# Kernel tuning notes

Measured on AMD Instinct MI355X. Metric: run time of the kernel, lower is better.

Reference implementation:

```python
import jax, jax.numpy as jnp
import numpy as np

N_NODES = 100000
N_EDGES = 1600000
D_FEAT = 64
NUM_LAYERS = 3


def setup_inputs() -> dict:
    key = jax.random.key(0)
    k1, k2, k3, k4 = jax.random.split(key, 4)
    X = jax.random.normal(k1, (N_NODES, D_FEAT), dtype=jnp.float32)
    src = jax.random.randint(k2, (N_EDGES,), 0, N_NODES, dtype=jnp.int32)
    dst = jax.random.randint(k3, (N_EDGES,), 0, N_NODES, dtype=jnp.int32)
    ew = jax.random.uniform(k4, (N_EDGES,), dtype=jnp.float32)
    return {"X": X, "src": src, "dst": dst, "ew": ew}


def _spmm(X, src, dst, ew):
    # gather source features, scale by edge weight, scatter-sum into dst
    msgs = X[src] * ew[:, None]  # [E, d]
    return jax.ops.segment_sum(msgs, dst, num_segments=N_NODES)


def reference(X, src, dst, ew):
    # LightGCNConv with stack_layers=True: average of layer-0..num_layers embeddings
    X_list = [X]
    h = X
    for _ in range(NUM_LAYERS):
        h = _spmm(h, src, dst, ew)
        X_list.append(h)
    return jnp.mean(jnp.stack(X_list, axis=1), axis=1)  # [N, d]
```

## Files before the change

kernel.cpp:

```cpp
#include <hip/hip_runtime.h>
#include <hip/hip_fp16.h>

#define N_NODES 100000
#define D_FEAT  64
#define N_EDGES 1600000
#define NPB     128
#define NBUCK   ((N_NODES + NPB - 1) / NPB)
#define CAP     3072
#define CVT_BLOCKS  500
#define CVT_THREADS 1024
#define CHUNK   (N_EDGES / CVT_BLOCKS)
#define PULL_BLOCKS 2048
#define WCAP    64

__global__ void init_bcur(int* __restrict__ bcur) {
    int t = threadIdx.x;
    if (t < NBUCK) bcur[t] = 0;
}

__global__ __launch_bounds__(CVT_THREADS) void cvt_part(const float* __restrict__ X,
                                                        __half* __restrict__ Xh,
                                                        const int* __restrict__ src,
                                                        const int* __restrict__ dst,
                                                        const float* __restrict__ ew,
                                                        int* __restrict__ bcur,
                                                        int2* __restrict__ edges_p) {
    __shared__ int h[NBUCK];
    const int t = threadIdx.x;
    for (int i = t; i < NBUCK; i += CVT_THREADS) h[i] = 0;

    const int n4 = N_NODES * D_FEAT / 4;
    for (int i = blockIdx.x * CVT_THREADS + t; i < n4; i += CVT_BLOCKS * CVT_THREADS) {
        float4 v = ((const float4*)X)[i];
        ((__half2*)Xh)[2 * i]     = __floats2half2_rn(v.x, v.y);
        ((__half2*)Xh)[2 * i + 1] = __floats2half2_rn(v.z, v.w);
    }
    __syncthreads();

    const int beg = blockIdx.x * CHUNK;
    const int base = beg + 4 * t;
    const bool act = (4 * t < CHUNK);

    int4 d4;
    if (act) {
        d4 = *(const int4*)(dst + base);
        atomicAdd(&h[d4.x >> 7], 1);
        atomicAdd(&h[d4.y >> 7], 1);
        atomicAdd(&h[d4.z >> 7], 1);
        atomicAdd(&h[d4.w >> 7], 1);
    }
    __syncthreads();

    if (t < NBUCK) {
        int c = h[t];
        h[t] = c ? atomicAdd(&bcur[t], c) : 0;
    }
    __syncthreads();

    if (act) {
        int4   s4 = *(const int4*)(src + base);
        float4 w4 = *(const float4*)(ew + base);
        int b, p;
        b = d4.x >> 7; p = atomicAdd(&h[b], 1);
        if (p < CAP) edges_p[(size_t)b * CAP + p] = make_int2(s4.x | ((d4.x & 127) << 17), __float_as_int(w4.x));
        b = d4.y >> 7; p = atomicAdd(&h[b], 1);
        if (p < CAP) edges_p[(size_t)b * CAP + p] = make_int2(s4.y | ((d4.y & 127) << 17), __float_as_int(w4.y));
        b = d4.z >> 7; p = atomicAdd(&h[b], 1);
        if (p < CAP) edges_p[(size_t)b * CAP + p] = make_int2(s4.z | ((d4.z & 127) << 17), __float_as_int(w4.z));
        b = d4.w >> 7; p = atomicAdd(&h[b], 1);
        if (p < CAP) edges_p[(size_t)b * CAP + p] = make_int2(s4.w | ((d4.w & 127) << 17), __float_as_int(w4.w));
    }
}

__global__ __launch_bounds__(256) void sort_bucket(const int2* __restrict__ edges_p,
                                                   const int* __restrict__ bcur,
                                                   int2* __restrict__ sedges,
                                                   int2* __restrict__ nodeptr) {
    __shared__ int cnt[NPB], sc[NPB], cur[NPB];
    __shared__ int2 buf[CAP];
    const int b = blockIdx.x, t = threadIdx.x;
    const int beg = b * CAP;
    int n = bcur[b];
    if (n > CAP) n = CAP;

    if (t < NPB) cnt[t] = 0;
    __syncthreads();
    for (int i = t; i < n; i += 256) {
        int2 e = edges_p[beg + i];
        buf[i] = e;
        atomicAdd(&cnt[e.x >> 17], 1);
    }
    __syncthreads();

    if (t < NPB) sc[t] = cnt[t];
    __syncthreads();
    for (int off = 1; off < NPB; off <<= 1) {
        int v = (t >= off && t < NPB) ? sc[t - off] : 0;
        __syncthreads();
        if (t < NPB) sc[t] += v;
        __syncthreads();
    }
    if (t < NPB) {
        cur[t] = sc[t] - cnt[t];
        int node = b * NPB + t;
        if (node < N_NODES) nodeptr[node] = make_int2(beg + sc[t] - cnt[t], cnt[t]);
    }
    __syncthreads();

    for (int i = t; i < n; i += 256) {
        int2 e = buf[i];
        int p = atomicAdd(&cur[e.x >> 17], 1);
        sedges[beg + p] = make_int2((e.x & 0x1FFFF) << 7, e.y);
    }
}

template <int MODE>
__global__ __launch_bounds__(256) void spmm_pull(const __half* __restrict__ hprev,
                                                 const int2* __restrict__ nodeptr,
                                                 const int2* __restrict__ edges,
                                                 __half* __restrict__ hout,
                                                 float* __restrict__ out,
                                                 const float* __restrict__ X,
                                                 const __half* __restrict__ h1,
                                                 const __half* __restrict__ h2) {
    __shared__ int2 ebuf[4][WCAP];
    const int t    = threadIdx.x;
    const int wid  = t >> 6;
    const int lane = t & 63;
    const int half = lane >> 5;
    const int sub  = lane & 31;
    const unsigned loff = 4u * sub;
    const int gw     = blockIdx.x * 4 + wid;
    const int nwaves = gridDim.x * 4;
    const char* hbase = (const char*)hprev;

    for (int node = gw; node < N_NODES; node += nwaves) {
        int2 np = nodeptr[node];
        const int beg = np.x, d = np.y;

        if (d <= WCAP) {
            const int dp = (d + 15) & ~15;
            if (lane < dp)
                ebuf[wid][lane] = (lane < d) ? edges[beg + lane] : make_int2(0, 0);
            float ax = 0.0f, ay = 0.0f;
            const int nb = dp >> 4;
            for (int bi = 0; bi < nb; ++bi) {
                const int base = bi * 16 + half;
                unsigned tv[8]; float w[8];
                #pragma unroll
                for (int k = 0; k < 8; ++k) {
                    int2 e = ebuf[wid][base + 2 * k];
                    w[k]  = __int_as_float(e.y);
                    tv[k] = *(const unsigned*)(hbase + ((unsigned)e.x + loff));
                }
                #pragma unroll
                for (int k = 0; k < 8; ++k) {
                    float2 f = __half22float2(*(__half2*)&tv[k]);
                    ax += f.x * w[k];
                    ay += f.y * w[k];
                }
            }
            ax += __shfl_xor(ax, 32);
            ay += __shfl_xor(ay, 32);
            if (half == 0) {
                size_t bo = (size_t)node * 32 + sub;
                if (MODE == 2) {
                    float2 x  = ((const float2*)X)[bo];
                    float2 f1 = __half22float2(((const __half2*)h1)[bo]);
                    float2 f2 = __half22float2(((const __half2*)h2)[bo]);
                    ((float2*)out)[bo] = make_float2((x.x + f1.x + f2.x + ax) * 0.25f,
                                                     (x.y + f1.y + f2.y + ay) * 0.25f);
                } else {
                    ((__half2*)hout)[bo] = __floats2half2_rn(ax, ay);
                }
            }
        } else {
            const int end = beg + d;
            float ax = 0.0f, ay = 0.0f;
            for (int j = beg; j < end; j += 16) {
                #pragma unroll
                for (int k = 0; k < 8; ++k) {
                    int idx = j + 2 * k + half;
                    int2 e = (idx < end) ? edges[idx] : make_int2(0, 0);
                    float wk = __int_as_float(e.y);
                    unsigned tvk = *(const unsigned*)(hbase + ((unsigned)e.x + loff));
                    float2 f = __half22float2(*(__half2*)&tvk);
                    ax += f.x * wk;
                    ay += f.y * wk;
                }
            }
            ax += __shfl_xor(ax, 32);
            ay += __shfl_xor(ay, 32);
            if (half == 0) {
                size_t bo = (size_t)node * 32 + sub;
                if (MODE == 2) {
                    float2 x  = ((const float2*)X)[bo];
                    float2 f1 = __half22float2(((const __half2*)h1)[bo]);
                    float2 f2 = __half22float2(((const __half2*)h2)[bo]);
                    ((float2*)out)[bo] = make_float2((x.x + f1.x + f2.x + ax) * 0.25f,
                                                     (x.y + f1.y + f2.y + ay) * 0.25f);
                } else {
                    ((__half2*)hout)[bo] = __floats2half2_rn(ax, ay);
                }
            }
        }
    }
}

extern "C" void kernel_launch(void* const* d_in, const int* in_sizes, int n_in,
                              void* d_out, int out_size, void* d_ws, size_t ws_size,
                              hipStream_t stream) {
    const float* X   = (const float*)d_in[0];
    const int*   src = (const int*)  d_in[1];
    const int*   dst = (const int*)  d_in[2];
    const float* ew  = (const float*)d_in[3];
    float* out = (float*)d_out;

    const size_t feat = (size_t)N_NODES * D_FEAT;

    char* p = (char*)d_ws;
    __half* hA      = (__half*)p; p += feat * sizeof(__half);
    __half* hB      = (__half*)p; p += feat * sizeof(__half);
    __half* Xh      = (__half*)p; p += feat * sizeof(__half);
    int2*  edges_p  = (int2*)p;   p += (size_t)NBUCK * CAP * sizeof(int2);
    int2*  sedges   = (int2*)p;   p += (size_t)NBUCK * CAP * sizeof(int2);
    int2*  nodeptr  = (int2*)p;   p += (size_t)N_NODES * sizeof(int2);
    int*   bcur     = (int*)p;    p += (size_t)NBUCK * 4;

    init_bcur  <<<1, 1024, 0, stream>>>(bcur);
    cvt_part   <<<CVT_BLOCKS, CVT_THREADS, 0, stream>>>(X, Xh, src, dst, ew, bcur, edges_p);
    sort_bucket<<<NBUCK, 256, 0, stream>>>(edges_p, bcur, sedges, nodeptr);

    spmm_pull<0><<<PULL_BLOCKS, 256, 0, stream>>>(Xh, nodeptr, sedges, hA, out, X, hA, hB);
    spmm_pull<1><<<PULL_BLOCKS, 256, 0, stream>>>(hA, nodeptr, sedges, hB, out, X, hA, hB);
    spmm_pull<2><<<PULL_BLOCKS, 256, 0, stream>>>(hB, nodeptr, sedges, (__half*)nullptr, out, X, hA, hB);
}
```

Measured before the change: 215.1 us.

## Fuse three SpMM layers into one cooperative kernel with grid syncs

Replaces the three separate spmm_pull launches with a single cooperative kernel that runs all three propagation layers, separated by grid-wide syncs, with the grid sized from occupancy (assuming 256 CUs). The aim is to remove kernel launch gaps and tail effects between layers. The sort_bucket block size also rises from 256 to 512 threads. Risks: grid.sync has its own cost, the occupancy-capped grid may give less parallelism than the old 2048 blocks, and the hardcoded CU count could exceed what can be co-resident, in which case the cooperative launch fails.

```diff
diff --git a/kernel.cpp b/kernel.cpp
--- a/kernel.cpp
+++ b/kernel.cpp
@@ -1,5 +1,8 @@
 #include <hip/hip_runtime.h>
 #include <hip/hip_fp16.h>
+#include <hip/hip_cooperative_groups.h>
+
+namespace cg = cooperative_groups;
 
 #define N_NODES 100000
 #define D_FEAT  64
@@ -72,10 +75,11 @@
     }
 }
 
-__global__ __launch_bounds__(256) void sort_bucket(const int2* __restrict__ edges_p,
-                                                   const int* __restrict__ bcur,
-                                                   int2* __restrict__ sedges,
-                                                   int2* __restrict__ nodeptr) {
+#define SORT_THREADS 512
+__global__ __launch_bounds__(SORT_THREADS) void sort_bucket(const int2* __restrict__ edges_p,
+                                                            const int* __restrict__ bcur,
+                                                            int2* __restrict__ sedges,
+                                                            int2* __restrict__ nodeptr) {
     __shared__ int cnt[NPB], sc[NPB], cur[NPB];
     __shared__ int2 buf[CAP];
     const int b = blockIdx.x, t = threadIdx.x;
@@ -85,7 +89,7 @@
 
     if (t < NPB) cnt[t] = 0;
     __syncthreads();
-    for (int i = t; i < n; i += 256) {
+    for (int i = t; i < n; i += SORT_THREADS) {
         int2 e = edges_p[beg + i];
         buf[i] = e;
         atomicAdd(&cnt[e.x >> 17], 1);
@@ -107,7 +111,7 @@
     }
     __syncthreads();
 
-    for (int i = t; i < n; i += 256) {
+    for (int i = t; i < n; i += SORT_THREADS) {
         int2 e = buf[i];
         int p = atomicAdd(&cur[e.x >> 17], 1);
         sedges[beg + p] = make_int2((e.x & 0x1FFFF) << 7, e.y);
@@ -115,15 +119,15 @@
 }
 
 template <int MODE>
-__global__ __launch_bounds__(256) void spmm_pull(const __half* __restrict__ hprev,
-                                                 const int2* __restrict__ nodeptr,
-                                                 const int2* __restrict__ edges,
-                                                 __half* __restrict__ hout,
-                                                 float* __restrict__ out,
-                                                 const float* __restrict__ X,
-                                                 const __half* __restrict__ h1,
-                                                 const __half* __restrict__ h2) {
-    __shared__ int2 ebuf[4][WCAP];
+__device__ __forceinline__ void spmm_body(const __half* __restrict__ hprev,
+                                          const int2* __restrict__ nodeptr,
+                                          const int2* __restrict__ edges,
+                                          __half* __restrict__ hout,
+                                          float* __restrict__ out,
+                                          const float* __restrict__ X,
+                                          const __half* __restrict__ h1,
+                                          const __half* __restrict__ h2,
+                                          int2 (&ebuf)[4][WCAP]) {
     const int t    = threadIdx.x;
     const int wid  = t >> 6;
     const int lane = t & 63;
@@ -207,6 +211,22 @@
     }
 }
 
+__global__ __launch_bounds__(256) void spmm_fused(const __half* __restrict__ Xh,
+                                                  const int2* __restrict__ nodeptr,
+                                                  const int2* __restrict__ sedges,
+                                                  __half* __restrict__ hA,
+                                                  __half* __restrict__ hB,
+                                                  float* __restrict__ out,
+                                                  const float* __restrict__ X) {
+    __shared__ int2 ebuf[4][WCAP];
+    cg::grid_group grid = cg::this_grid();
+    spmm_body<0>(Xh, nodeptr, sedges, hA, out, X, hA, hB, ebuf);
+    grid.sync();
+    spmm_body<1>(hA, nodeptr, sedges, hB, out, X, hA, hB, ebuf);
+    grid.sync();
+    spmm_body<2>(hB, nodeptr, sedges, (__half*)nullptr, out, X, hA, hB, ebuf);
+}
+
 extern "C" void kernel_launch(void* const* d_in, const int* in_sizes, int n_in,
                               void* d_out, int out_size, void* d_ws, size_t ws_size,
                               hipStream_t stream) {
@@ -229,9 +249,20 @@
 
     init_bcur  <<<1, 1024, 0, stream>>>(bcur);
     cvt_part   <<<CVT_BLOCKS, CVT_THREADS, 0, stream>>>(X, Xh, src, dst, ew, bcur, edges_p);
-    sort_bucket<<<NBUCK, 256, 0, stream>>>(edges_p, bcur, sedges, nodeptr);
-
-    spmm_pull<0><<<PULL_BLOCKS, 256, 0, stream>>>(Xh, nodeptr, sedges, hA, out, X, hA, hB);
-    spmm_pull<1><<<PULL_BLOCKS, 256, 0, stream>>>(hA, nodeptr, sedges, hB, out, X, hA, hB);
-    spmm_pull<2><<<PULL_BLOCKS, 256, 0, stream>>>(hB, nodeptr, sedges, (__half*)nullptr, out, X, hA, hB);
-}
+    sort_bucket<<<NBUCK, SORT_THREADS, 0, stream>>>(edges_p, bcur, sedges, nodeptr);
+
+    static int coop_blocks = 0;
+    if (coop_blocks == 0) {
+        int mb = 0;
+        hipError_t e = hipOccupancyMaxActiveBlocksPerMultiprocessor(&mb, (const void*)spmm_fused, 256, 0);
+        if (e != hipSuccess || mb <= 0) mb = 4;
+        if (mb > 8) mb = 8;
+        coop_blocks = mb * 256;
+        if (coop_blocks > PULL_BLOCKS) coop_blocks = PULL_BLOCKS;
+    }
+
+    void* args[] = {(void*)&Xh, (void*)&nodeptr, (void*)&sedges,
+                    (void*)&hA, (void*)&hB, (void*)&out, (void*)&X};
+    hipLaunchCooperativeKernel((const void*)spmm_fused, dim3(coop_blocks), dim3(256),
+                               args, 0, stream);
+}
```

Measured after the change: 485.2 us. 126% more time.

## Process node pairs per wave in SpMM pull and widen bucket sort blocks

Applied to the files above, without the earlier changes.

The pull kernel now handles two adjacent nodes per wavefront. Both nodes' edges are packed into one shared buffer when their padded degrees fit in 64, and each half-wave writes one node's result, so no half-wave sits idle during the store. Gathers for both nodes are issued together to raise memory-level parallelism. High-degree pairs fall back to the per-node loop. The sort kernel uses 512 threads, the bucket counter init kernel becomes a hipMemsetAsync, and launch bounds add an occupancy hint, which may force register limits.

```diff
diff --git a/kernel.cpp b/kernel.cpp
--- a/kernel.cpp
+++ b/kernel.cpp
@@ -11,12 +11,7 @@
 #define CVT_THREADS 1024
 #define CHUNK   (N_EDGES / CVT_BLOCKS)
 #define PULL_BLOCKS 2048
-#define WCAP    64
-
-__global__ void init_bcur(int* __restrict__ bcur) {
-    int t = threadIdx.x;
-    if (t < NBUCK) bcur[t] = 0;
-}
+#define SORT_THREADS 512
 
 __global__ __launch_bounds__(CVT_THREADS) void cvt_part(const float* __restrict__ X,
                                                         __half* __restrict__ Xh,
@@ -72,10 +67,10 @@
     }
 }
 
-__global__ __launch_bounds__(256) void sort_bucket(const int2* __restrict__ edges_p,
-                                                   const int* __restrict__ bcur,
-                                                   int2* __restrict__ sedges,
-                                                   int2* __restrict__ nodeptr) {
+__global__ __launch_bounds__(SORT_THREADS) void sort_bucket(const int2* __restrict__ edges_p,
+                                                            const int* __restrict__ bcur,
+                                                            int2* __restrict__ sedges,
+                                                            int2* __restrict__ nodeptr) {
     __shared__ int cnt[NPB], sc[NPB], cur[NPB];
     __shared__ int2 buf[CAP];
     const int b = blockIdx.x, t = threadIdx.x;
@@ -85,7 +80,7 @@
 
     if (t < NPB) cnt[t] = 0;
     __syncthreads();
-    for (int i = t; i < n; i += 256) {
+    for (int i = t; i < n; i += SORT_THREADS) {
         int2 e = edges_p[beg + i];
         buf[i] = e;
         atomicAdd(&cnt[e.x >> 17], 1);
@@ -107,7 +102,7 @@
     }
     __syncthreads();
 
-    for (int i = t; i < n; i += 256) {
+    for (int i = t; i < n; i += SORT_THREADS) {
         int2 e = buf[i];
         int p = atomicAdd(&cur[e.x >> 17], 1);
         sedges[beg + p] = make_int2((e.x & 0x1FFFF) << 7, e.y);
@@ -115,15 +110,15 @@
 }
 
 template <int MODE>
-__global__ __launch_bounds__(256) void spmm_pull(const __half* __restrict__ hprev,
-                                                 const int2* __restrict__ nodeptr,
-                                                 const int2* __restrict__ edges,
-                                                 __half* __restrict__ hout,
-                                                 float* __restrict__ out,
-                                                 const float* __restrict__ X,
-                                                 const __half* __restrict__ h1,
-                                                 const __half* __restrict__ h2) {
-    __shared__ int2 ebuf[4][WCAP];
+__global__ __launch_bounds__(256, 8) void spmm_pull(const __half* __restrict__ hprev,
+                                                    const int2* __restrict__ nodeptr,
+                                                    const int2* __restrict__ edges,
+                                                    __half* __restrict__ hout,
+                                                    float* __restrict__ out,
+                                                    const float* __restrict__ X,
+                                                    const __half* __restrict__ h1,
+                                                    const __half* __restrict__ h2) {
+    __shared__ int2 ebuf[4][64];
     const int t    = threadIdx.x;
     const int wid  = t >> 6;
     const int lane = t & 63;
@@ -133,74 +128,117 @@
     const int gw     = blockIdx.x * 4 + wid;
     const int nwaves = gridDim.x * 4;
     const char* hbase = (const char*)hprev;
-
-    for (int node = gw; node < N_NODES; node += nwaves) {
-        int2 np = nodeptr[node];
-        const int beg = np.x, d = np.y;
-
-        if (d <= WCAP) {
-            const int dp = (d + 15) & ~15;
-            if (lane < dp)
-                ebuf[wid][lane] = (lane < d) ? edges[beg + lane] : make_int2(0, 0);
-            float ax = 0.0f, ay = 0.0f;
-            const int nb = dp >> 4;
+    const int npairs = N_NODES >> 1;
+
+    for (int pr = gw; pr < npairs; pr += nwaves) {
+        const int nodeA = pr * 2;
+        const int2 npA = nodeptr[nodeA];
+        const int2 npB = nodeptr[nodeA + 1];
+        const int dA = npA.y, dB = npB.y;
+        const int padA = (dA + 15) & ~15;
+        const int padB = (dB + 15) & ~15;
+
+        if (padA + padB <= 64) {
+            {
+                int2 ev = make_int2(0, 0);
+                if (lane < padA) {
+                    if (lane < dA) ev = edges[npA.x + lane];
+                } else if (lane < padA + padB) {
+                    int j = lane - padA;
+                    if (j < dB) ev = edges[npB.x + j];
+                }
+                if (lane < padA + padB) ebuf[wid][lane] = ev;
+            }
+            float axA = 0.f, ayA = 0.f, axB = 0.f, ayB = 0.f;
+            const int nbA = padA >> 4, nbB = padB >> 4;
+            const int nb = (nbA > nbB) ? nbA : nbB;
             for (int bi = 0; bi < nb; ++bi) {
-                const int base = bi * 16 + half;
-                unsigned tv[8]; float w[8];
-                #pragma unroll
-                for (int k = 0; k < 8; ++k) {
-                    int2 e = ebuf[wid][base + 2 * k];
-                    w[k]  = __int_as_float(e.y);
-                    tv[k] = *(const unsigned*)(hbase + ((unsigned)e.x + loff));
-                }
-                #pragma unroll
-                for (int k = 0; k < 8; ++k) {
-                    float2 f = __half22float2(*(__half2*)&tv[k]);
-                    ax += f.x * w[k];
-                    ay += f.y * w[k];
-                }
-            }
-            ax += __shfl_xor(ax, 32);
-            ay += __shfl_xor(ay, 32);
-            if (half == 0) {
-                size_t bo = (size_t)node * 32 + sub;
-                if (MODE == 2) {
-                    float2 x  = ((const float2*)X)[bo];
-                    float2 f1 = __half22float2(((const __half2*)h1)[bo]);
-                    float2 f2 = __half22float2(((const __half2*)h2)[bo]);
-                    ((float2*)out)[bo] = make_float2((x.x + f1.x + f2.x + ax) * 0.25f,
-                                                     (x.y + f1.y + f2.y + ay) * 0.25f);
-                } else {
-                    ((__half2*)hout)[bo] = __floats2half2_rn(ax, ay);
-                }
+                unsigned tvA[8], tvB[8];
+                float wA[8], wB[8];
+                const bool doA = bi < nbA, doB = bi < nbB;
+                if (doA) {
+                    const int baseA = bi * 16 + half;
+                    #pragma unroll
+                    for (int k = 0; k < 8; ++k) {
+                        int2 e = ebuf[wid][baseA + 2 * k];
+                        wA[k]  = __int_as_float(e.y);
+                        tvA[k] = *(const unsigned*)(hbase + ((unsigned)e.x + loff));
+                    }
+                }
+                if (doB) {
+                    const int baseB = padA + bi * 16 + half;
+                    #pragma unroll
+                    for (int k = 0; k < 8; ++k) {
+                        int2 e = ebuf[wid][baseB + 2 * k];
+                        wB[k]  = __int_as_float(e.y);
+                        tvB[k] = *(const unsigned*)(hbase + ((unsigned)e.x + loff));
+                    }
+                }
+                if (doA) {
+                    #pragma unroll
+                    for (int k = 0; k < 8; ++k) {
+                        float2 f = __half22float2(*(__half2*)&tvA[k]);
+                        axA += f.x * wA[k];
+                        ayA += f.y * wA[k];
+                    }
+                }
+                if (doB) {
+                    #pragma unroll
+                    for (int k = 0; k < 8; ++k) {
+                        float2 f = __half22float2(*(__half2*)&tvB[k]);
+                        axB += f.x * wB[k];
+                        ayB += f.y * wB[k];
+                    }
+                }
+            }
+            axA += __shfl_xor(axA, 32); ayA += __shfl_xor(ayA, 32);
+            axB += __shfl_xor(axB, 32); ayB += __shfl_xor(ayB, 32);
+            const int node = nodeA + half;
+            const float ax = half ? axB : axA;
+            const float ay = half ? ayB : ayA;
+            size_t bo = (size_t)node * 32 + sub;
+            if (MODE == 2) {
+                float2 x  = ((const float2*)X)[bo];
+                float2 f1 = __half22float2(((const __half2*)h1)[bo]);
+                float2 f2 = __half22float2(((const __half2*)h2)[bo]);
+                ((float2*)out)[bo] = make_float2((x.x + f1.x + f2.x + ax) * 0.25f,
+                                                 (x.y + f1.y + f2.y + ay) * 0.25f);
+            } else {
+                ((__half2*)hout)[bo] = __floats2half2_rn(ax, ay);
             }
         } else {
-            const int end = beg + d;
-            float ax = 0.0f, ay = 0.0f;
-            for (int j = beg; j < end; j += 16) {
-                #pragma unroll
-                for (int k = 0; k < 8; ++k) {
-                    int idx = j + 2 * k + half;
-                    int2 e = (idx < end) ? edges[idx] : make_int2(0, 0);
-                    float wk = __int_as_float(e.y);
-                    unsigned tvk = *(const unsigned*)(hbase + ((unsigned)e.x + loff));
-                    float2 f = __half22float2(*(__half2*)&tvk);
-                    ax += f.x * wk;
-                    ay += f.y * wk;
-                }
-            }
-            ax += __shfl_xor(ax, 32);
-            ay += __shfl_xor(ay, 32);
-            if (half == 0) {
-                size_t bo = (size_t)node * 32 + sub;
-                if (MODE == 2) {
-                    float2 x  = ((const float2*)X)[bo];
-                    float2 f1 = __half22float2(((const __half2*)h1)[bo]);
-                    float2 f2 = __half22float2(((const __half2*)h2)[bo]);
-                    ((float2*)out)[bo] = make_float2((x.x + f1.x + f2.x + ax) * 0.25f,
-                                                     (x.y + f1.y + f2.y + ay) * 0.25f);
-                } else {
-                    ((__half2*)hout)[bo] = __floats2half2_rn(ax, ay);
+            #pragma unroll 1
+            for (int s = 0; s < 2; ++s) {
+                const int node = nodeA + s;
+                const int beg = s ? npB.x : npA.x;
+                const int d   = s ? dB : dA;
+                const int end = beg + d;
+                float ax = 0.f, ay = 0.f;
+                for (int j = beg; j < end; j += 16) {
+                    #pragma unroll
+                    for (int k = 0; k < 8; ++k) {
+                        int idx = j + 2 * k + half;
+                        int2 e = (idx < end) ? edges[idx] : make_int2(0, 0);
+                        float wk = __int_as_float(e.y);
+                        unsigned tvk = *(const unsigned*)(hbase + ((unsigned)e.x + loff));
+                        float2 f = __half22float2(*(__half2*)&tvk);
+                        ax += f.x * wk;
+                        ay += f.y * wk;
+                    }
+                }
+                ax += __shfl_xor(ax, 32);
+                ay += __shfl_xor(ay, 32);
+                if (half == 0) {
+                    size_t bo = (size_t)node * 32 + sub;
+                    if (MODE == 2) {
+                        float2 x  = ((const float2*)X)[bo];
+                        float2 f1 = __half22float2(((const __half2*)h1)[bo]);
+                        float2 f2 = __half22float2(((const __half2*)h2)[bo]);
+                        ((float2*)out)[bo] = make_float2((x.x + f1.x + f2.x + ax) * 0.25f,
+                                                         (x.y + f1.y + f2.y + ay) * 0.25f);
+                    } else {
+                        ((__half2*)hout)[bo] = __floats2half2_rn(ax, ay);
+                    }
                 }
             }
         }
@@ -227,9 +265,10 @@
     int2*  nodeptr  = (int2*)p;   p += (size_t)N_NODES * sizeof(int2);
     int*   bcur     = (int*)p;    p += (size_t)NBUCK * 4;
 
-    init_bcur  <<<1, 1024, 0, stream>>>(bcur);
+    hipMemsetAsync(bcur, 0, (size_t)NBUCK * sizeof(int), stream);
+
     cvt_part   <<<CVT_BLOCKS, CVT_THREADS, 0, stream>>>(X, Xh, src, dst, ew, bcur, edges_p);
-    sort_bucket<<<NBUCK, 256, 0, stream>>>(edges_p, bcur, sedges, nodeptr);
+    sort_bucket<<<NBUCK, SORT_THREADS, 0, stream>>>(edges_p, bcur, sedges, nodeptr);
 
     spmm_pull<0><<<PULL_BLOCKS, 256, 0, stream>>>(Xh, nodeptr, sedges, hA, out, X, hA, hB);
     spmm_pull<1><<<PULL_BLOCKS, 256, 0, stream>>>(hA, nodeptr, sedges, hB, out, X, hA, hB);
```

Result: slower. 362.8 us (+68.6%).

## Fuse bucket sort with first SpMM layer using shared-memory edge lists

Applied to the files above, without the earlier changes.

Merges the per-bucket counting sort and the first-layer pull SpMM into one kernel. The sorted edges stay in LDS, padded per node to multiples of 16, so layer 0 reads them from shared memory instead of global. This drops one kernel launch and one global round trip of the sorted edges. It also replaces the init kernel with hipMemsetAsync. In exchange it uses 512 threads and about 37KB of LDS per block, which may lower occupancy, and each bucket's layer-0 work is serialized within one block.

```diff
diff --git a/kernel.cpp b/kernel.cpp
--- a/kernel.cpp
+++ b/kernel.cpp
@@ -7,16 +7,12 @@
 #define NPB     128
 #define NBUCK   ((N_NODES + NPB - 1) / NPB)
 #define CAP     3072
+#define PCAP    4608
 #define CVT_BLOCKS  500
 #define CVT_THREADS 1024
 #define CHUNK   (N_EDGES / CVT_BLOCKS)
 #define PULL_BLOCKS 2048
 #define WCAP    64
-
-__global__ void init_bcur(int* __restrict__ bcur) {
-    int t = threadIdx.x;
-    if (t < NBUCK) bcur[t] = 0;
-}
 
 __global__ __launch_bounds__(CVT_THREADS) void cvt_part(const float* __restrict__ X,
                                                         __half* __restrict__ Xh,
@@ -72,45 +68,116 @@
     }
 }
 
-__global__ __launch_bounds__(256) void sort_bucket(const int2* __restrict__ edges_p,
-                                                   const int* __restrict__ bcur,
-                                                   int2* __restrict__ sedges,
-                                                   int2* __restrict__ nodeptr) {
-    __shared__ int cnt[NPB], sc[NPB], cur[NPB];
-    __shared__ int2 buf[CAP];
+__global__ __launch_bounds__(512) void sort_pull0(const int2* __restrict__ edges_p,
+                                                  const int* __restrict__ bcur,
+                                                  int2* __restrict__ sedges,
+                                                  int2* __restrict__ nodeptr,
+                                                  const __half* __restrict__ Xh,
+                                                  __half* __restrict__ hA) {
+    __shared__ int cnt[NPB], usc[NPB], psc[NPB], cur[NPB];
+    __shared__ int2 sbuf[PCAP];
+    __shared__ int fits;
     const int b = blockIdx.x, t = threadIdx.x;
-    const int beg = b * CAP;
+    const int gbeg = b * CAP;
     int n = bcur[b];
     if (n > CAP) n = CAP;
 
     if (t < NPB) cnt[t] = 0;
     __syncthreads();
-    for (int i = t; i < n; i += 256) {
-        int2 e = edges_p[beg + i];
-        buf[i] = e;
-        atomicAdd(&cnt[e.x >> 17], 1);
-    }
-    __syncthreads();
-
-    if (t < NPB) sc[t] = cnt[t];
+    for (int i = t; i < n; i += 512)
+        atomicAdd(&cnt[edges_p[gbeg + i].x >> 17], 1);
+    __syncthreads();
+
+    if (t < NPB) { usc[t] = cnt[t]; psc[t] = (cnt[t] + 15) & ~15; }
     __syncthreads();
     for (int off = 1; off < NPB; off <<= 1) {
-        int v = (t >= off && t < NPB) ? sc[t - off] : 0;
+        int u = 0, p = 0;
+        if (t >= off && t < NPB) { u = usc[t - off]; p = psc[t - off]; }
         __syncthreads();
-        if (t < NPB) sc[t] += v;
+        if (t < NPB) { usc[t] += u; psc[t] += p; }
         __syncthreads();
     }
+    if (t == NPB - 1) fits = (psc[t] <= PCAP);
     if (t < NPB) {
-        cur[t] = sc[t] - cnt[t];
+        cur[t] = usc[t] - cnt[t];
         int node = b * NPB + t;
-        if (node < N_NODES) nodeptr[node] = make_int2(beg + sc[t] - cnt[t], cnt[t]);
-    }
-    __syncthreads();
-
-    for (int i = t; i < n; i += 256) {
-        int2 e = buf[i];
-        int p = atomicAdd(&cur[e.x >> 17], 1);
-        sedges[beg + p] = make_int2((e.x & 0x1FFFF) << 7, e.y);
+        if (node < N_NODES) nodeptr[node] = make_int2(gbeg + usc[t] - cnt[t], cnt[t]);
+    }
+    __syncthreads();
+    const bool padded = (fits != 0);
+
+    for (int i = t; i < n; i += 512) {
+        int2 e = edges_p[gbeg + i];
+        int node = e.x >> 17;
+        int r = atomicAdd(&cur[node], 1);
+        int rank = r - (usc[node] - cnt[node]);
+        int2 v = make_int2((e.x & 0x1FFFF) << 7, e.y);
+        sedges[gbeg + r] = v;
+        int lb = padded ? (psc[node] - ((cnt[node] + 15) & ~15)) : (usc[node] - cnt[node]);
+        sbuf[lb + rank] = v;
+    }
+    if (padded) {
+        int node = t >> 2, j = t & 3;
+        int c = cnt[node], pd = (c + 15) & ~15;
+        int lb = psc[node] - pd;
+        for (int s = c + j; s < pd; s += 4) sbuf[lb + s] = make_int2(0, 0);
+    }
+    __syncthreads();
+
+    const int wid  = t >> 6;
+    const int lane = t & 63;
+    const int half = lane >> 5;
+    const int sub  = lane & 31;
+    const unsigned loff = 4u * sub;
+    const char* hbase = (const char*)Xh;
+
+    for (int w = 0; w < 16; ++w) {
+        const int li = wid * 16 + w;
+        const int node = b * NPB + li;
+        if (node >= N_NODES) break;
+        const int c = cnt[li];
+        float ax = 0.f, ay = 0.f;
+        if (padded) {
+            const int pd = (c + 15) & ~15;
+            const int lb = psc[li] - pd;
+            const int nb = pd >> 4;
+            for (int bi = 0; bi < nb; ++bi) {
+                const int base = lb + bi * 16 + half;
+                unsigned tv[8]; float wk[8];
+                #pragma unroll
+                for (int k = 0; k < 8; ++k) {
+                    int2 e = sbuf[base + 2 * k];
+                    wk[k] = __int_as_float(e.y);
+                    tv[k] = *(const unsigned*)(hbase + ((unsigned)e.x + loff));
+                }
+                #pragma unroll
+                for (int k = 0; k < 8; ++k) {
+                    float2 f = __half22float2(*(__half2*)&tv[k]);
+                    ax += f.x * wk[k];
+                    ay += f.y * wk[k];
+                }
+            }
+        } else {
+            const int lb = usc[li] - c;
+            for (int j = 0; j < c; j += 16) {
+                #pragma unroll
+                for (int k = 0; k < 8; ++k) {
+                    int idx = j + 2 * k + half;
+                    int2 e = (idx < c) ? sbuf[lb + idx] : make_int2(0, 0);
+                    float wv = __int_as_float(e.y);
+                    unsigned tvk = *(const unsigned*)(hbase + ((unsigned)e.x + loff));
+                    float2 f = __half22float2(*(__half2*)&tvk);
+                    ax += f.x * wv;
+                    ay += f.y * wv;
+                }
+            }
+        }
+        ax += __shfl_xor(ax, 32);
+        ay += __shfl_xor(ay, 32);
+        if (half == 0) {
+            size_t bo = (size_t)node * 32 + sub;
+            ((__half2*)hA)[bo] = __floats2half2_rn(ax, ay);
+        }
     }
 }
 
@@ -227,11 +294,11 @@
     int2*  nodeptr  = (int2*)p;   p += (size_t)N_NODES * sizeof(int2);
     int*   bcur     = (int*)p;    p += (size_t)NBUCK * 4;
 
-    init_bcur  <<<1, 1024, 0, stream>>>(bcur);
-    cvt_part   <<<CVT_BLOCKS, CVT_THREADS, 0, stream>>>(X, Xh, src, dst, ew, bcur, edges_p);
-    sort_bucket<<<NBUCK, 256, 0, stream>>>(edges_p, bcur, sedges, nodeptr);
-
-    spmm_pull<0><<<PULL_BLOCKS, 256, 0, stream>>>(Xh, nodeptr, sedges, hA, out, X, hA, hB);
+    hipMemsetAsync(bcur, 0, (size_t)NBUCK * sizeof(int), stream);
+
+    cvt_part  <<<CVT_BLOCKS, CVT_THREADS, 0, stream>>>(X, Xh, src, dst, ew, bcur, edges_p);
+    sort_pull0<<<NBUCK, 512, 0, stream>>>(edges_p, bcur, sedges, nodeptr, Xh, hA);
+
     spmm_pull<1><<<PULL_BLOCKS, 256, 0, stream>>>(hA, nodeptr, sedges, hB, out, X, hA, hB);
     spmm_pull<2><<<PULL_BLOCKS, 256, 0, stream>>>(hB, nodeptr, sedges, (__half*)nullptr, out, X, hA, hB);
 }
```

Measured after the change: 221.2 us. +2.8%, slower.
